# Optimization experiments

Hardware: AMD Instinct MI355X
Metric: run time of the kernel (lower is better)

Reference implementation:

```python
import jax, jax.numpy as jnp
import numpy as np

D_L = 64
HIDDEN = 64
CUBE = (D_L + 1) ** 3  # 274625


def setup_inputs() -> dict:
    key = jax.random.key(0)
    ks = jax.random.split(key, 9)
    B = 512
    l = jax.random.normal(ks[0], (B, D_L), dtype=jnp.float32)
    a = jax.random.normal(ks[1], (B, D_L), dtype=jnp.float32)
    v = jax.random.normal(ks[2], (B, D_L), dtype=jnp.float32)
    # Linear params (xavier-ish scale)
    W1 = jax.random.normal(ks[3], (CUBE, HIDDEN), dtype=jnp.float32) * (1.0 / np.sqrt(CUBE))
    b1 = jnp.zeros((HIDDEN,), dtype=jnp.float32)
    W2 = jax.random.normal(ks[4], (HIDDEN, HIDDEN), dtype=jnp.float32) * (1.0 / np.sqrt(HIDDEN))
    b2 = jnp.zeros((HIDDEN,), dtype=jnp.float32)
    W3 = jax.random.normal(ks[5], (HIDDEN, D_L), dtype=jnp.float32) * (1.0 / np.sqrt(HIDDEN))
    b3 = jnp.zeros((D_L,), dtype=jnp.float32)
    return {"l": l, "a": a, "v": v, "W1": W1, "b1": b1, "W2": W2, "b2": b2, "W3": W3, "b3": b3}


def reference(l, a, v, W1, b1, W2, b2, W3, b3):
    B = a.shape[0]
    ones = jnp.ones((B, 1), dtype=a.dtype)
    a_h = jnp.concatenate([ones, a], axis=1)  # [B, d+1]
    v_h = jnp.concatenate([ones, v], axis=1)
    t_h = jnp.concatenate([ones, l], axis=1)
    # fusion[b, i, j, k] = a_h[b,i] * v_h[b,j] * t_h[b,k]; flattened row-major (i,j,k)
    fusion = jnp.einsum('bi,bj,bk->bijk', a_h, v_h, t_h).reshape(B, -1)  # [B, (d+1)^3]
    h = jnp.tanh(fusion @ W1 + b1)
    h = jnp.tanh(h @ W2 + b2)
    out = jnp.tanh(h @ W3 + b3)
    return out
```

## Files before the change

### kernel.cpp

```cpp
#include <hip/hip_runtime.h>
#include <hip/hip_fp16.h>


typedef _Float16 f16;
typedef f16 f16x8 __attribute__((ext_vector_type(8)));
typedef f16 f16x2 __attribute__((ext_vector_type(2)));
typedef float fx4 __attribute__((ext_vector_type(4)));
typedef unsigned int u32;

#define WS_AT    0
#define WS_VT    131072
#define WS_PART  262144

__device__ __forceinline__ void load_lds16(const float* g, float* lds) {
  __builtin_amdgcn_global_load_lds((const __attribute__((address_space(1))) u32*)g,
                                   (__attribute__((address_space(3))) u32*)lds, 16, 0, 0);
}

__device__ __forceinline__ void seg_decode(int s, int& ia, int& iv, int& isel,
                                           int& rowbase, int& rowstride) {
  if (s < 4096)      { int i = s >> 6, j = s & 63; ia = i; iv = j; isel = 0;
                       rowbase = (i+1)*4225 + (j+1)*65 + 1; rowstride = 1; }
  else if (s < 4160) { int i = s - 4096; ia = i; iv = -1; isel = 2;
                       rowbase = (i+1)*4225 + 65; rowstride = 65; }
  else if (s < 4224) { int i = s - 4160; ia = i; iv = -1; isel = 0;
                       rowbase = (i+1)*4225 + 1; rowstride = 1; }
  else if (s < 4288) { int j = s - 4224; ia = -1; iv = j; isel = 0;
                       rowbase = (j+1)*65 + 1; rowstride = 1; }
  else if (s == 4288){ ia = -1; iv = -1; isel = 1; rowbase = 4225; rowstride = 4225; }
  else if (s == 4289){ ia = -1; iv = -1; isel = 2; rowbase = 65;   rowstride = 65; }
  else if (s == 4290){ ia = -1; iv = -1; isel = 0; rowbase = 1;    rowstride = 1; }
  else               { ia = -2; iv = -1; isel = 0; rowbase = 1;    rowstride = 1; }
}

__device__ __forceinline__ f16x8 cvt8(fx4 x0, fx4 x1) {
  f16x8 f;
  f[0]=(f16)x0[0]; f[1]=(f16)x0[1]; f[2]=(f16)x0[2]; f[3]=(f16)x0[3];
  f[4]=(f16)x1[0]; f[5]=(f16)x1[1]; f[6]=(f16)x1[2]; f[7]=(f16)x1[3];
  return f;
}
__device__ __forceinline__ f16x8 cvt8s(float a0,float a1,float a2,float a3,
                                       float a4,float a5,float a6,float a7){
  f16x8 f; f[0]=(f16)a0; f[1]=(f16)a1; f[2]=(f16)a2; f[3]=(f16)a3;
  f[4]=(f16)a4; f[5]=(f16)a5; f[6]=(f16)a6; f[7]=(f16)a7; return f;
}

__global__ __launch_bounds__(256) void prep_kernel(
    const float* __restrict__ a, const float* __restrict__ v,
    float* __restrict__ aT, float* __restrict__ vT)
{
  int g = blockIdx.x * 256 + threadIdx.x;
  int which = g >> 15;
  int idx = g & 32767;
  if (which == 0) aT[idx] = a[((idx & 511) << 6) + (idx >> 9)];
  else            vT[idx] = v[((idx & 511) << 6) + (idx >> 9)];
}

__global__ __launch_bounds__(256, 2) void fusion_gemm(
    const float* __restrict__ W1,
    const float* __restrict__ aT, const float* __restrict__ vT,
    const float* __restrict__ a, const float* __restrict__ v, const float* __restrict__ l,
    f16* __restrict__ partials)
{
  __shared__ float sbuf[4][4096];
  __shared__ f16 pl_all[17][256];

  const int tid  = threadIdx.x;
  const int bid  = blockIdx.x;
  const int grp  = bid >> 4;
  const int rr   = bid & 15;
  const int half = rr >> 3;
  const int slot = rr & 7;
  const int chunk = (grp << 3) + slot;
  const int lane = tid & 63;
  const int wave = tid >> 6;
  const int l15  = lane & 15;
  const int l4   = lane >> 4;
  const int segbase = chunk * 17;
  const int row0 = half << 8;

  #pragma unroll
  for (int t = 0; t < 17; ++t) {
    int s = segbase + t, ia, iv, is_, rb, rs;
    seg_decode(s, ia, iv, is_, rb, rs);
    float spa = (ia >= 0) ? aT[(ia << 9) + row0 + tid] : (ia == -1 ? 1.0f : 0.0f);
    float spv = (iv >= 0) ? vT[(iv << 9) + row0 + tid] : 1.0f;
    pl_all[t][tid] = (f16)(spa * spv);
  }

  f16x8 lfrag[4][2], vfrag[4][2];
  #pragma unroll
  for (int mt = 0; mt < 4; ++mt) {
    int row = row0 + (wave << 6) + (mt << 4) + l15;
    #pragma unroll
    for (int ks = 0; ks < 2; ++ks) {
      const float* pl_ = l + (row << 6) + (ks << 5) + (l4 << 3);
      lfrag[mt][ks] = cvt8(*(const fx4*)pl_, *(const fx4*)(pl_ + 4));
      const float* pv_ = v + (row << 6) + (ks << 5) + (l4 << 3);
      vfrag[mt][ks] = cvt8(*(const fx4*)pv_, *(const fx4*)(pv_ + 4));
    }
  }

  fx4 acc[4][4] = {};

#define STAGE(T, BUF) do {                                                   \
    int s_ = segbase + (T), ia_, iv_, is_, rb_, rs_;                         \
    seg_decode(s_, ia_, iv_, is_, rb_, rs_);                                 \
    _Pragma("unroll")                                                        \
    for (int h_ = 0; h_ < 4; ++h_) {                                         \
      int c_  = (h_ << 8) + (wave << 6) + lane;                              \
      int k_  = c_ >> 4;                                                     \
      int n4_ = ((c_ & 15) - 2 * (k_ >> 3)) & 15;                            \
      const float* g_ = W1 + (size_t)(rb_ + k_ * rs_) * 64 + (n4_ << 2);     \
      load_lds16(g_, &sbuf[BUF][((h_ << 8) + (wave << 6)) << 2]);            \
    }                                                                        \
  } while (0)

  asm volatile("s_waitcnt lgkmcnt(0)\n\ts_barrier" ::: "memory");

  STAGE(0, 0); STAGE(1, 1); STAGE(2, 2);

  #pragma unroll 1
  for (int t = 0; t < 17; ++t) {
    if (t < 15)       asm volatile("s_waitcnt vmcnt(8)\n\ts_barrier" ::: "memory");
    else if (t == 15) asm volatile("s_waitcnt vmcnt(4)\n\ts_barrier" ::: "memory");
    else              asm volatile("s_waitcnt vmcnt(0)\n\ts_barrier" ::: "memory");
    __builtin_amdgcn_sched_barrier(0);

    if (t + 3 < 17) {
      switch ((t + 3) & 3) {
        case 0: STAGE(t + 3, 0); break;
        case 1: STAGE(t + 3, 1); break;
        case 2: STAGE(t + 3, 2); break;
        case 3: STAGE(t + 3, 3); break;
      }
    }

    int s = segbase + t;
    int isel = ((s >= 4096 && s < 4160) || s == 4289) ? 2 : (s == 4288 ? 1 : 0);
    const float* bufc = sbuf[t & 3];

    __builtin_amdgcn_s_setprio(1);
    #pragma unroll
    for (int ks = 0; ks < 2; ++ks) {
      f16x8 bf[4];
      #pragma unroll
      for (int nt = 0; nt < 4; ++nt) {
        int n = (nt << 4) + l15;
        int col4 = ((n >> 2) + 2 * ((ks << 2) + l4)) & 15;
        int dw = (((ks << 5) + (l4 << 3)) << 6) + (col4 << 2) + (n & 3);
        bf[nt] = cvt8s(bufc[dw],       bufc[dw + 64],  bufc[dw + 128], bufc[dw + 192],
                       bufc[dw + 256], bufc[dw + 320], bufc[dw + 384], bufc[dw + 448]);
      }
      #pragma unroll
      for (int mt = 0; mt < 4; ++mt) {
        int lrow = (wave << 6) + (mt << 4) + l15;
        f16 ps = pl_all[t][lrow];
        f16x8 lv;
        if (isel == 0)      lv = lfrag[mt][ks];
        else if (isel == 2) lv = vfrag[mt][ks];
        else { const float* p_ = a + ((row0 + lrow) << 6) + (ks << 5) + (l4 << 3);
               lv = cvt8(*(const fx4*)p_, *(const fx4*)(p_ + 4)); }
        f16x2 ps2 = { ps, ps };
        f16x8 av;
        ((f16x2*)&av)[0] = ((f16x2*)&lv)[0] * ps2;
        ((f16x2*)&av)[1] = ((f16x2*)&lv)[1] * ps2;
        ((f16x2*)&av)[2] = ((f16x2*)&lv)[2] * ps2;
        ((f16x2*)&av)[3] = ((f16x2*)&lv)[3] * ps2;
        #pragma unroll
        for (int nt = 0; nt < 4; ++nt)
          acc[mt][nt] = __builtin_amdgcn_mfma_f32_16x16x32_f16(av, bf[nt], acc[mt][nt], 0, 0, 0);
      }
    }
    __builtin_amdgcn_s_setprio(0);
  }
#undef STAGE

  #pragma unroll
  for (int mt = 0; mt < 4; ++mt)
    #pragma unroll
    for (int nt = 0; nt < 4; ++nt)
      #pragma unroll
      for (int r = 0; r < 4; ++r) {
        int grow = row0 + (wave << 6) + (mt << 4) + (l4 << 2) + r;
        int col = (nt << 4) + l15;
        partials[((size_t)grow << 14) + (chunk << 6) + col] = (f16)acc[mt][nt][r];
      }
}

__global__ __launch_bounds__(256) void tail_kernel(
    const f16* __restrict__ partials, const float* __restrict__ W1, const float* __restrict__ b1,
    const float* __restrict__ W2, const float* __restrict__ b2,
    const float* __restrict__ W3, const float* __restrict__ b3, float* __restrict__ out)
{
  __shared__ float red[256][8];
  __shared__ float hbuf[64];
  __shared__ float h2buf[64];
  const int row = blockIdx.x;
  const int t = threadIdx.x;
  const f16* base = partials + ((size_t)row << 14);

  float s[8] = {0.f,0.f,0.f,0.f,0.f,0.f,0.f,0.f};
  #pragma unroll
  for (int j = 0; j < 8; ++j) {
    f16x8 vv = *(const f16x8*)(base + (((j << 8) + t) << 3));
    #pragma unroll
    for (int e = 0; e < 8; ++e) s[e] += (float)vv[e];
  }
  #pragma unroll
  for (int e = 0; e < 8; ++e) red[t][e] = s[e];
  __syncthreads();
  if (t < 64) {
    float acc = b1[t] + W1[t];
    #pragma unroll
    for (int k = 0; k < 32; ++k) acc += red[(t >> 3) + (k << 3)][t & 7];
    hbuf[t] = tanhf(acc);
  }
  __syncthreads();
  if (t < 64) {
    float acc = b2[t];
    #pragma unroll 8
    for (int k = 0; k < 64; ++k) acc += hbuf[k] * W2[(k << 6) + t];
    h2buf[t] = tanhf(acc);
  }
  __syncthreads();
  if (t < 64) {
    float acc = b3[t];
    #pragma unroll 8
    for (int k = 0; k < 64; ++k) acc += h2buf[k] * W3[(k << 6) + t];
    out[(row << 6) + t] = tanhf(acc);
  }
}

extern "C" void kernel_launch(void* const* d_in, const int* in_sizes, int n_in,
                              void* d_out, int out_size, void* d_ws, size_t ws_size,
                              hipStream_t stream) {
  const float* l  = (const float*)d_in[0];
  const float* a  = (const float*)d_in[1];
  const float* v  = (const float*)d_in[2];
  const float* W1 = (const float*)d_in[3];
  const float* b1 = (const float*)d_in[4];
  const float* W2 = (const float*)d_in[5];
  const float* b2 = (const float*)d_in[6];
  const float* W3 = (const float*)d_in[7];
  const float* b3 = (const float*)d_in[8];
  float* out = (float*)d_out;

  char* ws = (char*)d_ws;
  float* aT = (float*)(ws + WS_AT);
  float* vT = (float*)(ws + WS_VT);
  f16* partials = (f16*)(ws + WS_PART);

  hipLaunchKernelGGL(prep_kernel, dim3(256), dim3(256), 0, stream, a, v, aT, vT);
  hipLaunchKernelGGL(fusion_gemm, dim3(512), dim3(256), 0, stream,
                     W1, aT, vT, a, v, l, partials);
  hipLaunchKernelGGL(tail_kernel, dim3(512), dim3(256), 0, stream,
                     partials, W1, b1, W2, b2, W3, b3, out);
}
```

Baseline: 62.80 us.

## Load W1 fragments directly from global into registers instead of LDS pipeline

Removes the 4-stage global_load_lds LDS ring buffer and its waitcnt/barrier scheduling. Each wave now reads its W1 B-fragments straight from global memory into registers and converts them with packed round-toward-zero cvt_pkrtz. The A-side scaled fragments are precomputed once per segment. This drops LDS traffic and per-iteration barriers, but loses the explicit prefetch overlap, and every wave now redundantly issues uncoalesced scalar global loads for the same W1 tile.

```diff
diff --git a/kernel.cpp b/kernel.cpp
--- a/kernel.cpp
+++ b/kernel.cpp
@@ -5,16 +5,16 @@
 typedef _Float16 f16;
 typedef f16 f16x8 __attribute__((ext_vector_type(8)));
 typedef f16 f16x2 __attribute__((ext_vector_type(2)));
+typedef __fp16 fp16x2 __attribute__((ext_vector_type(2)));
 typedef float fx4 __attribute__((ext_vector_type(4)));
-typedef unsigned int u32;
 
 #define WS_AT    0
 #define WS_VT    131072
 #define WS_PART  262144
 
-__device__ __forceinline__ void load_lds16(const float* g, float* lds) {
-  __builtin_amdgcn_global_load_lds((const __attribute__((address_space(1))) u32*)g,
-                                   (__attribute__((address_space(3))) u32*)lds, 16, 0, 0);
+__device__ __forceinline__ f16x2 pkrtz(float a, float b) {
+  fp16x2 r = __builtin_amdgcn_cvt_pkrtz(a, b);
+  return *(f16x2*)&r;
 }
 
 __device__ __forceinline__ void seg_decode(int s, int& ia, int& iv, int& isel,
@@ -39,11 +39,6 @@
   f[4]=(f16)x1[0]; f[5]=(f16)x1[1]; f[6]=(f16)x1[2]; f[7]=(f16)x1[3];
   return f;
 }
-__device__ __forceinline__ f16x8 cvt8s(float a0,float a1,float a2,float a3,
-                                       float a4,float a5,float a6,float a7){
-  f16x8 f; f[0]=(f16)a0; f[1]=(f16)a1; f[2]=(f16)a2; f[3]=(f16)a3;
-  f[4]=(f16)a4; f[5]=(f16)a5; f[6]=(f16)a6; f[7]=(f16)a7; return f;
-}
 
 __global__ __launch_bounds__(256) void prep_kernel(
     const float* __restrict__ a, const float* __restrict__ v,
@@ -62,7 +57,6 @@
     const float* __restrict__ a, const float* __restrict__ v, const float* __restrict__ l,
     f16* __restrict__ partials)
 {
-  __shared__ float sbuf[4][4096];
   __shared__ f16 pl_all[17][256];
 
   const int tid  = threadIdx.x;
@@ -103,78 +97,69 @@
 
   fx4 acc[4][4] = {};
 
-#define STAGE(T, BUF) do {                                                   \
-    int s_ = segbase + (T), ia_, iv_, is_, rb_, rs_;                         \
-    seg_decode(s_, ia_, iv_, is_, rb_, rs_);                                 \
-    _Pragma("unroll")                                                        \
-    for (int h_ = 0; h_ < 4; ++h_) {                                         \
-      int c_  = (h_ << 8) + (wave << 6) + lane;                              \
-      int k_  = c_ >> 4;                                                     \
-      int n4_ = ((c_ & 15) - 2 * (k_ >> 3)) & 15;                            \
-      const float* g_ = W1 + (size_t)(rb_ + k_ * rs_) * 64 + (n4_ << 2);     \
-      load_lds16(g_, &sbuf[BUF][((h_ << 8) + (wave << 6)) << 2]);            \
-    }                                                                        \
-  } while (0)
-
-  asm volatile("s_waitcnt lgkmcnt(0)\n\ts_barrier" ::: "memory");
-
-  STAGE(0, 0); STAGE(1, 1); STAGE(2, 2);
+  __syncthreads();
 
   #pragma unroll 1
   for (int t = 0; t < 17; ++t) {
-    if (t < 15)       asm volatile("s_waitcnt vmcnt(8)\n\ts_barrier" ::: "memory");
-    else if (t == 15) asm volatile("s_waitcnt vmcnt(4)\n\ts_barrier" ::: "memory");
-    else              asm volatile("s_waitcnt vmcnt(0)\n\ts_barrier" ::: "memory");
-    __builtin_amdgcn_sched_barrier(0);
-
-    if (t + 3 < 17) {
-      switch ((t + 3) & 3) {
-        case 0: STAGE(t + 3, 0); break;
-        case 1: STAGE(t + 3, 1); break;
-        case 2: STAGE(t + 3, 2); break;
-        case 3: STAGE(t + 3, 3); break;
-      }
-    }
-
-    int s = segbase + t;
-    int isel = ((s >= 4096 && s < 4160) || s == 4289) ? 2 : (s == 4288 ? 1 : 0);
-    const float* bufc = sbuf[t & 3];
-
-    __builtin_amdgcn_s_setprio(1);
-    #pragma unroll
-    for (int ks = 0; ks < 2; ++ks) {
-      f16x8 bf[4];
-      #pragma unroll
-      for (int nt = 0; nt < 4; ++nt) {
-        int n = (nt << 4) + l15;
-        int col4 = ((n >> 2) + 2 * ((ks << 2) + l4)) & 15;
-        int dw = (((ks << 5) + (l4 << 3)) << 6) + (col4 << 2) + (n & 3);
-        bf[nt] = cvt8s(bufc[dw],       bufc[dw + 64],  bufc[dw + 128], bufc[dw + 192],
-                       bufc[dw + 256], bufc[dw + 320], bufc[dw + 384], bufc[dw + 448]);
-      }
-      #pragma unroll
-      for (int mt = 0; mt < 4; ++mt) {
-        int lrow = (wave << 6) + (mt << 4) + l15;
-        f16 ps = pl_all[t][lrow];
+    int s = segbase + t, ia_, iv_, isel, rb, rs;
+    seg_decode(s, ia_, iv_, isel, rb, rs);
+
+    f16x8 av[4][2];
+    #pragma unroll
+    for (int mt = 0; mt < 4; ++mt) {
+      int lrow = (wave << 6) + (mt << 4) + l15;
+      f16 ps = pl_all[t][lrow];
+      f16x2 ps2 = { ps, ps };
+      #pragma unroll
+      for (int ks = 0; ks < 2; ++ks) {
         f16x8 lv;
         if (isel == 0)      lv = lfrag[mt][ks];
         else if (isel == 2) lv = vfrag[mt][ks];
-        else { const float* p_ = a + ((row0 + lrow) << 6) + (ks << 5) + (l4 << 3);
+        else { const float* p_ = a + ((size_t)(row0 + lrow) << 6) + (ks << 5) + (l4 << 3);
                lv = cvt8(*(const fx4*)p_, *(const fx4*)(p_ + 4)); }
-        f16x2 ps2 = { ps, ps };
-        f16x8 av;
-        ((f16x2*)&av)[0] = ((f16x2*)&lv)[0] * ps2;
-        ((f16x2*)&av)[1] = ((f16x2*)&lv)[1] * ps2;
-        ((f16x2*)&av)[2] = ((f16x2*)&lv)[2] * ps2;
-        ((f16x2*)&av)[3] = ((f16x2*)&lv)[3] * ps2;
-        #pragma unroll
-        for (int nt = 0; nt < 4; ++nt)
-          acc[mt][nt] = __builtin_amdgcn_mfma_f32_16x16x32_f16(av, bf[nt], acc[mt][nt], 0, 0, 0);
+        ((f16x2*)&av[mt][ks])[0] = ((f16x2*)&lv)[0] * ps2;
+        ((f16x2*)&av[mt][ks])[1] = ((f16x2*)&lv)[1] * ps2;
+        ((f16x2*)&av[mt][ks])[2] = ((f16x2*)&lv)[2] * ps2;
+        ((f16x2*)&av[mt][ks])[3] = ((f16x2*)&lv)[3] * ps2;
       }
     }
-    __builtin_amdgcn_s_setprio(0);
-  }
-#undef STAGE
+
+    float w[2][4][8];
+    if (rs == 1) {
+      const float* b0 = W1 + (((size_t)(rb + (l4 << 3))) << 6) + l15;
+      const float* b1 = b0 + (32 << 6);
+      #pragma unroll
+      for (int nt = 0; nt < 4; ++nt)
+        #pragma unroll
+        for (int e = 0; e < 8; ++e) {
+          w[0][nt][e] = b0[(nt << 4) + (e << 6)];
+          w[1][nt][e] = b1[(nt << 4) + (e << 6)];
+        }
+    } else {
+      #pragma unroll
+      for (int ks = 0; ks < 2; ++ks)
+        #pragma unroll
+        for (int nt = 0; nt < 4; ++nt) {
+          const float* b = W1 + (size_t)(rb + ((ks << 5) + (l4 << 3)) * rs) * 64 + (nt << 4) + l15;
+          #pragma unroll
+          for (int e = 0; e < 8; ++e) w[ks][nt][e] = b[(size_t)(e * rs) << 6];
+        }
+    }
+
+    #pragma unroll
+    for (int ks = 0; ks < 2; ++ks)
+      #pragma unroll
+      for (int nt = 0; nt < 4; ++nt) {
+        f16x8 bf;
+        ((f16x2*)&bf)[0] = pkrtz(w[ks][nt][0], w[ks][nt][1]);
+        ((f16x2*)&bf)[1] = pkrtz(w[ks][nt][2], w[ks][nt][3]);
+        ((f16x2*)&bf)[2] = pkrtz(w[ks][nt][4], w[ks][nt][5]);
+        ((f16x2*)&bf)[3] = pkrtz(w[ks][nt][6], w[ks][nt][7]);
+        #pragma unroll
+        for (int mt = 0; mt < 4; ++mt)
+          acc[mt][nt] = __builtin_amdgcn_mfma_f32_16x16x32_f16(av[mt][ks], bf, acc[mt][nt], 0, 0, 0);
+      }
+  }
 
   #pragma unroll
   for (int mt = 0; mt < 4; ++mt)
```

Result: slower. 73.81 us (+17.5%).
